# Optimization experiments

Hardware: AMD Instinct MI355X
Metric: run time of the kernel (lower is better)

Reference implementation:

```python
import jax, jax.numpy as jnp
import numpy as np

H_DIM = 256
N_HEADS = 8
HALF = H_DIM // 2

def _lin(x, W, b):
    # torch nn.Linear: y = x @ W.T + b
    y = x @ W.T
    return y + b if b is not None else y

def setup_inputs() -> dict:
    key = jax.random.key(0)
    ks = jax.random.split(key, 16)
    s = 0.02
    d = {
        'x': jax.random.normal(ks[0], (16, H_DIM, 32, 32), jnp.float32),
        'q1_w': jax.random.normal(ks[1], (HALF, HALF), jnp.float32) * s,
        'q1_b': jnp.zeros((HALF,), jnp.float32),
        'q2_w': jax.random.normal(ks[2], (HALF, HALF), jnp.float32) * s,
        'q2_b': jnp.zeros((HALF,), jnp.float32),
        'k1_w': jax.random.normal(ks[3], (HALF, HALF), jnp.float32) * s,
        'k1_b': jnp.zeros((HALF,), jnp.float32),
        'k2_w': jax.random.normal(ks[4], (HALF, HALF), jnp.float32) * s,
        'k2_b': jnp.zeros((HALF,), jnp.float32),
        'v1_w': jax.random.normal(ks[5], (HALF, HALF), jnp.float32) * s,
        'v1_b': jnp.zeros((HALF,), jnp.float32),
        'v2_w': jax.random.normal(ks[6], (HALF, HALF), jnp.float32) * s,
        'v2_b': jnp.zeros((HALF,), jnp.float32),
        'proj1_w': jax.random.normal(ks[7], (HALF, HALF), jnp.float32) * s,
        'proj1_b': jnp.zeros((HALF,), jnp.float32),
        'proj2_w': jax.random.normal(ks[8], (HALF, HALF), jnp.float32) * s,
        'proj2_b': jnp.zeros((HALF,), jnp.float32),
        'logit_scale': jnp.log(10.0 * jnp.ones((N_HEADS, 1, 1), jnp.float32)),
        'mlp_w1': jax.random.normal(ks[9], (128, 2), jnp.float32) * s,
        'mlp_b1': jnp.zeros((128,), jnp.float32),
        'mlp_w2': jax.random.normal(ks[10], (N_HEADS, 128), jnp.float32) * s,
    }
    return d

def _rel_pos_index(h, w):
    # static (numpy) relative position index, shape [N, N]
    ch, cw = np.meshgrid(np.arange(h), np.arange(w), indexing='ij')
    coords = np.stack([ch.reshape(-1), cw.reshape(-1)])  # [2, N]
    rel = coords[:, :, None] - coords[:, None, :]         # [2, N, N]
    rel = rel.transpose(1, 2, 0)
    rel[:, :, 0] += h - 1
    rel[:, :, 1] += w - 1
    return rel[:, :, 0] * (2 * w - 1) + rel[:, :, 1]

def _forward(x, q1_w, q1_b, q2_w, q2_b, k1_w, k1_b, k2_w, k2_b,
             v1_w, v1_b, v2_w, v2_b, proj1_w, proj1_b, proj2_w, proj2_b,
             logit_scale, mlp_w1, mlp_b1, mlp_w2):
    b, c, h, w = x.shape
    N = h * w
    nh = N_HEADS
    hd = c // nh
    x3 = jnp.transpose(x, (0, 2, 3, 1)).reshape(b, N, c)
    x0, x1 = x3[..., :c // 2], x3[..., c // 2:]

    def qkv(W0, b0, W1, b1):
        t = jnp.concatenate([x0 + _lin(x0, W0, b0), x1 + _lin(x1, W1, b1)], axis=-1)
        return t.reshape(b, N, nh, hd).transpose(0, 2, 1, 3)  # [b, nh, N, hd]

    q = qkv(q1_w, q1_b, q2_w, q2_b)
    k = qkv(k1_w, k1_b, k2_w, k2_b)
    v = qkv(v1_w, v1_b, v2_w, v2_b)

    eps = 1e-12
    qn = q / jnp.maximum(jnp.linalg.norm(q, axis=-1, keepdims=True), eps)
    kn = k / jnp.maximum(jnp.linalg.norm(k, axis=-1, keepdims=True), eps)
    attn = jnp.einsum('bhnd,bhmd->bhnm', qn, kn)  # cosine similarity
    scale = jnp.exp(jnp.minimum(logit_scale, jnp.log(1.0 / 0.01)))  # [nh,1,1]
    attn = attn * scale[None]

    # continuous relative-position bias (CPB) table via small MLP
    rch = jnp.arange(-(h - 1), h, dtype=jnp.float32) / (h - 1 + 1e-8)
    rcw = jnp.arange(-(w - 1), w, dtype=jnp.float32) / (w - 1 + 1e-8)
    gh, gw = jnp.meshgrid(rch, rcw, indexing='ij')
    tab = jnp.stack([gh, gw], axis=-1) * 3.2               # [2h-1, 2w-1, 2]
    tab = jnp.sign(tab) * (1.0 - jnp.exp(-jnp.abs(tab)))
    tab = jax.nn.relu(_lin(tab, mlp_w1, mlp_b1))
    tab = _lin(tab, mlp_w2, None).reshape(-1, nh)          # [(2h-1)(2w-1), nh]

    idx = jnp.asarray(_rel_pos_index(h, w))                # [N, N]
    bias = tab[idx.reshape(-1)].reshape(N, N, nh).transpose(2, 0, 1)
    bias = 16.0 * jax.nn.sigmoid(bias)
    attn = attn + bias[None]

    attn = jax.nn.softmax(attn, axis=-1)
    out = jnp.einsum('bhnm,bhmd->bhnd', attn, v).transpose(0, 2, 1, 3).reshape(b, N, c)
    o0, o1 = out[..., :c // 2], out[..., c // 2:]
    out = jnp.concatenate([_lin(o0, proj1_w, proj1_b), _lin(o1, proj2_w, proj2_b)], axis=-1)
    return out.reshape(b, h, w, c).transpose(0, 3, 1, 2)

def reference(x, q1_w, q1_b, q2_w, q2_b, k1_w, k1_b, k2_w, k2_b,
              v1_w, v1_b, v2_w, v2_b, proj1_w, proj1_b, proj2_w, proj2_b,
              logit_scale, mlp_w1, mlp_b1, mlp_w2):
    return _forward(x, q1_w, q1_b, q2_w, q2_b, k1_w, k1_b, k2_w, k2_b,
                    v1_w, v1_b, v2_w, v2_b, proj1_w, proj1_b, proj2_w, proj2_b,
                    logit_scale, mlp_w1, mlp_b1, mlp_w2)
```

## Files before the change

kernel.cpp:

```cpp
#include <hip/hip_runtime.h>
#include <cmath>


typedef _Float16 half_t;
typedef __attribute__((ext_vector_type(2))) __fp16 fp16x2;
typedef __attribute__((ext_vector_type(4))) _Float16 half4;
typedef __attribute__((ext_vector_type(8))) _Float16 half8;
typedef __attribute__((ext_vector_type(2))) float float2v;
typedef __attribute__((ext_vector_type(4))) float float4v;
typedef __attribute__((ext_vector_type(2))) unsigned int uint2v;

static __device__ __forceinline__ float4v mfma16(half8 a, half8 b, float4v c) {
  return __builtin_amdgcn_mfma_f32_16x16x32_f16(a, b, c, 0, 0, 0);
}

struct PtrArr8 { const float* p[8]; };

__global__ __launch_bounds__(256) void prep_w(PtrArr8 wsrc, PtrArr8 bsrc,
                                              half_t* __restrict__ wf,
                                              float* __restrict__ bws) {
  int y = blockIdx.y;
  const float* src = nullptr;
  const float* bs = nullptr;
#pragma unroll
  for (int i = 0; i < 8; i++)
    if (i == y) { src = wsrc.p[i]; bs = bsrc.p[i]; }
  int flat = (blockIdx.x * 256 + threadIdx.x) * 4;
  float4 w = *(const float4*)(src + flat);
  int j = flat >> 7, k = flat & 127;
  if (y < 6) {
    if (k == j)     w.x += 1.0f;
    if (k + 1 == j) w.y += 1.0f;
    if (k + 2 == j) w.z += 1.0f;
    if (k + 3 == j) w.w += 1.0f;
  }
  half4 h;
  h[0] = (half_t)w.x;
  h[1] = (half_t)w.y;
  h[2] = (half_t)w.z;
  h[3] = (half_t)w.w;
  int ng = j >> 4, l = j & 15, ks = k >> 5, quad = (k >> 3) & 3, o8 = k & 7;
  *(half4*)(wf + y * 16384 + ((ng * 4 + ks) * 64 + quad * 16 + l) * 8 + o8) =
      h;
  if (blockIdx.x == 0 && threadIdx.x < 128)
    bws[y * 128 + threadIdx.x] = bs[threadIdx.x];
}

__global__ __launch_bounds__(256) void bias_mlp(const float* __restrict__ w1,
                                                const float* __restrict__ b1,
                                                const float* __restrict__ w2,
                                                const float* __restrict__ ls,
                                                float* __restrict__ tabh2) {
  __shared__ float sw1[256];
  __shared__ float sb1[128];
  __shared__ float sw2[1024];
  int t = threadIdx.x;
  sw1[t] = w1[t];
  if (t < 128) sb1[t] = b1[t];
  for (int i = t; i < 1024; i += 256) sw2[i] = w2[i];
  __syncthreads();
  int p = blockIdx.x * 256 + t;
  if (p >= 3969) return;
  int ph = p / 63, pw = p % 63;
  float t0 = (float)(ph - 31) * (3.2f / 31.0f);
  float t1 = (float)(pw - 31) * (3.2f / 31.0f);
  t0 = copysignf(1.0f - __expf(-fabsf(t0)), t0);
  t1 = copysignf(1.0f - __expf(-fabsf(t1)), t1);
  float acc[8];
#pragma unroll
  for (int hh = 0; hh < 8; hh++) acc[hh] = 0.0f;
  for (int j = 0; j < 128; j++) {
    float hj = fmaxf(0.0f, t0 * sw1[2 * j] + t1 * sw1[2 * j + 1] + sb1[j]);
#pragma unroll
    for (int hh = 0; hh < 8; hh++) acc[hh] += hj * sw2[hh * 128 + j];
  }
  const float L2E = 1.44269504f;
#pragma unroll
  for (int hh = 0; hh < 8; hh++) {
    float scale = __expf(fminf(ls[hh], 4.6051702f));
    float c14 = 14.0f - (scale + 16.0f) * L2E;
    float bias = 16.0f / (1.0f + __expf(-acc[hh]));
    tabh2[hh * 3969 + p] = bias * L2E + c14;
  }
}

__global__ __launch_bounds__(256, 4) void qkv_mfma(
    const float* __restrict__ x, const half_t* __restrict__ wfrag,
    const float* __restrict__ lscale, const float* __restrict__ bws,
    half_t* __restrict__ qf, half_t* __restrict__ kf,
    half_t* __restrict__ vf) {
  __shared__ half_t tbuf[4608];
  int t = threadIdx.x;
  int lane = t & 63, wv = t >> 6, l = lane & 15, quad = lane >> 4;
  int rw = wv & 1, cw = wv >> 1;
  int hf = blockIdx.y;
  int m0 = blockIdx.x * 32;
  int b = m0 >> 10, n0 = m0 & 1023;

  half8 afr[4];
  {
    const float* xb =
        x + ((size_t)b * 256 + hf * 128) * 1024 + n0 + rw * 16 + l;
#pragma unroll
    for (int ks = 0; ks < 4; ks++) {
      half8 a;
#pragma unroll
      for (int j = 0; j < 8; j++)
        a[j] = (half_t)xb[(size_t)(ks * 32 + quad * 8 + j) * 1024];
      afr[ks] = a;
    }
  }

  for (int op = 0; op < 3; op++) {
    int combo = op * 2 + hf;
    const half_t* wfb = wfrag + combo * 16384;
    float4v acc[4];
#pragma unroll
    for (int ngl = 0; ngl < 4; ngl++) {
      int ng = cw * 4 + ngl;
      float4v c = {0.f, 0.f, 0.f, 0.f};
#pragma unroll
      for (int ks = 0; ks < 4; ks++) {
        half8 bfrag =
            *(const half8*)(wfb + ((ng * 4 + ks) * 64 + lane) * 8);
        c = mfma16(afr[ks], bfrag, c);
      }
      acc[ngl] = c;
    }
#pragma unroll
    for (int ngl = 0; ngl < 4; ngl++) {
      float bb = bws[combo * 128 + (cw * 4 + ngl) * 16 + l];
#pragma unroll
      for (int r2 = 0; r2 < 4; r2++) acc[ngl][r2] += bb;
    }
    if (op < 2) {
#pragma unroll
      for (int hgl = 0; hgl < 2; hgl++) {
        float sc = 1.0f;
        if (op == 0)
          sc = __expf(fminf(lscale[hf * 4 + cw * 2 + hgl], 4.6051702f)) *
               1.44269504f;
#pragma unroll
        for (int r2 = 0; r2 < 4; r2++) {
          float ss = acc[2 * hgl][r2] * acc[2 * hgl][r2] +
                     acc[2 * hgl + 1][r2] * acc[2 * hgl + 1][r2];
          ss += __shfl_xor(ss, 1, 64);
          ss += __shfl_xor(ss, 2, 64);
          ss += __shfl_xor(ss, 4, 64);
          ss += __shfl_xor(ss, 8, 64);
          float rn = sc / fmaxf(sqrtf(ss), 1e-12f);
          acc[2 * hgl][r2] *= rn;
          acc[2 * hgl + 1][r2] *= rn;
        }
      }
#pragma unroll
      for (int ngl = 0; ngl < 4; ngl++)
#pragma unroll
        for (int r2 = 0; r2 < 4; r2++)
          tbuf[(rw * 16 + quad * 4 + r2) * 136 + (cw * 4 + ngl) * 16 + l] =
              (half_t)acc[ngl][r2];
      __syncthreads();
      half_t* dst = (op == 0) ? qf : kf;
#pragma unroll
      for (int i = 0; i < 2; i++) {
        int idx = t + 256 * i;
        int row = idx >> 4, colc = (idx & 15) * 8;
        half8 vv = *(const half8*)(tbuf + row * 136 + colc);
        int head = hf * 4 + (colc >> 5), d = colc & 31;
        *(half8*)(dst + (((size_t)b * 8 + head) * 1024 + n0 + row) * 32 + d) =
            vv;
      }
      __syncthreads();
    } else {
#pragma unroll
      for (int ngl = 0; ngl < 4; ngl++) {
        int col = (cw * 4 + ngl) * 16 + l;
        half4 hv;
#pragma unroll
        for (int r2 = 0; r2 < 4; r2++) hv[r2] = (half_t)acc[ngl][r2];
        *(half4*)(tbuf + col * 36 + rw * 16 + quad * 4) = hv;
      }
      __syncthreads();
#pragma unroll
      for (int i = 0; i < 8; i++) {
        int idx = t + 256 * i;
        int col = idx >> 4, rp = idx & 15;
        unsigned int val = *(const unsigned int*)(tbuf + col * 36 + rp * 2);
        int head = hf * 4 + (col >> 5);
        int d = col & 31;
        *(unsigned int*)((char*)vf +
                         (((((size_t)b * 8 + head) * 32 + d) * 1024) + n0 +
                          rp * 2) * 2) = val;
      }
    }
  }
}


#define LOADKV(kt, VV)                                                      \
  {                                                                         \
    _Pragma("unroll") for (int nt = 0; nt < 4; nt++)                        \
        kfr[nt] = *(const half8*)(kbase + ((kt)*64 + nt * 16 + l) * 32 +    \
                                  quad * 8);                                \
    _Pragma("unroll") for (int ks = 0; ks < 2; ks++) {                      \
      VV[0][ks] = *(const half8*)(vbase + l * 1024 + (kt)*64 + ks * 32 +    \
                                  quad * 8);                                \
      VV[1][ks] = *(const half8*)(vbase + (16 + l) * 1024 + (kt)*64 +       \
                                  ks * 32 + quad * 8);                      \
    }                                                                       \
  }

#define QK_PHASE(kt, S, SR)                                                 \
  {                                                                         \
    int rowb = (wv + 31 - 2 * (kt)) * 63 + cA + (S)*16;                     \
    _Pragma("unroll") for (int nt = 0; nt < 4; nt++) {                      \
      int base = rowb - (nt >> 1) * 63 - (nt & 1) * 16;                     \
      float2v p0 = sb2d[base];                                              \
      float2v p1 = sb2d[base - 2];                                          \
      float4v c;                                                            \
      c[0] = p0[1];                                                         \
      c[1] = p0[0];                                                         \
      c[2] = p1[1];                                                         \
      c[3] = p1[0];                                                         \
      SR[nt] = mfma16(kfr[nt], qfr[S], c);                                  \
    }                                                                       \
  }

#define EXP_WRITE(S, SR)                                                    \
  {                                                                         \
    half_t* paws = pa + (wv * 2 + (S)) * 1152;                              \
    _Pragma("unroll") for (int nt = 0; nt < 4; nt++) {                      \
      fp16x2 plo = __builtin_amdgcn_cvt_pkrtz(exp2f(SR[nt][0]),             \
                                              exp2f(SR[nt][1]));            \
      fp16x2 phi = __builtin_amdgcn_cvt_pkrtz(exp2f(SR[nt][2]),             \
                                              exp2f(SR[nt][3]));            \
      uint2v uu;                                                            \
      uu.x = __builtin_bit_cast(unsigned int, plo);                         \
      uu.y = __builtin_bit_cast(unsigned int, phi);                         \
      *(uint2v*)(paws + l * 72 +                                            \
                 (((nt * 2 + (quad >> 1)) ^ pswz) << 3) +                   \
                 ((quad & 1) << 2)) = uu;                                   \
    }                                                                       \
  }

#define PV_PHASE(S, VV)                                                     \
  {                                                                         \
    const half_t* paws = pa + (wv * 2 + (S)) * 1152;                        \
    _Pragma("unroll") for (int ks = 0; ks < 2; ks++) {                      \
      half8 pfr = *(const half8*)(paws + l * 72 +                           \
                                  (((ks * 4 + quad) ^ pswz) << 3));         \
      o0[S] = mfma16(pfr, VV[0][ks], o0[S]);                                \
      o1[S] = mfma16(pfr, VV[1][ks], o1[S]);                                \
      accl[S] = mfma16(pfr, ones, accl[S]);                                 \
    }                                                                       \
  }

#define ITER(kt, VC, VN, DO_PREV, DO_PREF)                                  \
  {                                                                         \
    float4v sres[4];                                                        \
    QK_PHASE(kt, 0, sres);                                                  \
    if (DO_PREV) PV_PHASE(1, VN);                                           \
    EXP_WRITE(0, sres);                                                     \
    float4v sres2[4];                                                       \
    QK_PHASE(kt, 1, sres2);                                                 \
    if (DO_PREF) LOADKV((kt) + 1, VN);                                      \
    PV_PHASE(0, VC);                                                        \
    EXP_WRITE(1, sres2);                                                    \
  }

__global__ __launch_bounds__(256) void attn_mfma(
    const half_t* __restrict__ qf, const half_t* __restrict__ kf,
    const half_t* __restrict__ vf, const float* __restrict__ tabh2,
    half_t* __restrict__ ao) {
  __shared__ float2v sb2d[2205];
  __shared__ half_t pa[9216];

  int id = blockIdx.x;
  int qo = id >> 7;
  int bh = id & 127;
  int h = bh & 7, b = bh >> 3;
  int t = threadIdx.x;
  int lane = t & 63, wv = t >> 6, l = lane & 15, quad = lane >> 4;
  size_t bhs = (size_t)b * 8 + h;
  const half_t* kbase = kf + bhs * 1024 * 32;
  const half_t* vbase = vf + bhs * 32 * 1024;
  int row0 = qo * 128 + wv * 32;
  int cA = l + 31 - quad * 4;
  int pswz = (l >> 3) << 2;

  half8 kfr[4], va[2][2], vb[2][2], qfr[2];
  LOADKV(0, va);
#pragma unroll
  for (int s = 0; s < 2; s++)
    qfr[s] = *(const half8*)(qf + (bhs * 1024 + row0 + s * 16 + l) * 32 +
                             quad * 8);

  {
    const float* tb = tabh2 + h * 3969 + qo * 252;
    for (int i = t; i < 2205; i += 256) {
      float2v pr;
      pr[0] = (i > 0) ? tb[i - 1] : 0.0f;
      pr[1] = tb[i];
      sb2d[i] = pr;
    }
  }

  float4v o0[2], o1[2], accl[2];
#pragma unroll
  for (int s = 0; s < 2; s++) {
    o0[s] = (float4v){0.f, 0.f, 0.f, 0.f};
    o1[s] = (float4v){0.f, 0.f, 0.f, 0.f};
    accl[s] = (float4v){0.f, 0.f, 0.f, 0.f};
  }
  half8 ones;
#pragma unroll
  for (int j = 0; j < 8; j++) ones[j] = (half_t)1.0f;

  __syncthreads();

  ITER(0, va, vb, 0, 1);
  ITER(1, vb, va, 1, 1);
  for (int kt2 = 2; kt2 < 14; kt2 += 2) {
    ITER(kt2, va, vb, 1, 1);
    ITER(kt2 + 1, vb, va, 1, 1);
  }
  ITER(14, va, vb, 1, 1);
  ITER(15, vb, va, 1, 0);
  PV_PHASE(1, vb);

#pragma unroll
  for (int s = 0; s < 2; s++) {
#pragma unroll
    for (int r2 = 0; r2 < 4; r2++) {
      float linv = 1.0f / accl[s][r2];
      size_t rowaddr =
          ((size_t)b * 1024 + row0 + s * 16 + quad * 4 + r2) * 256 + h * 32;
      ao[rowaddr + l] = (half_t)(o0[s][r2] * linv);
      ao[rowaddr + 16 + l] = (half_t)(o1[s][r2] * linv);
    }
  }
}

__global__ __launch_bounds__(256, 4) void proj_mfma(
    const half_t* __restrict__ ao, const half_t* __restrict__ wfrag,
    const float* __restrict__ bws, float* __restrict__ out) {
  __shared__ float yt[128 * 36];
  int t = threadIdx.x;
  int lane = t & 63, wv = t >> 6, l = lane & 15, quad = lane >> 4;
  int rw = wv & 1, cw = wv >> 1;
  int hf = blockIdx.y;
  int m0 = blockIdx.x * 32;
  int b = m0 >> 10, n0 = m0 & 1023;

  half8 afr[4];
  const half_t* ab =
      ao + ((size_t)m0 + rw * 16 + l) * 256 + hf * 128 + quad * 8;
#pragma unroll
  for (int ks = 0; ks < 4; ks++) afr[ks] = *(const half8*)(ab + ks * 32);

  const half_t* wfb = wfrag + (6 + hf) * 16384;
#pragma unroll
  for (int ngl = 0; ngl < 4; ngl++) {
    int ng = cw * 4 + ngl;
    float4v c = {0.f, 0.f, 0.f, 0.f};
#pragma unroll
    for (int ks = 0; ks < 4; ks++) {
      half8 bfrag = *(const half8*)(wfb + ((ng * 4 + ks) * 64 + lane) * 8);
      c = mfma16(afr[ks], bfrag, c);
    }
    float bb = bws[(6 + hf) * 128 + ng * 16 + l];
#pragma unroll
    for (int r2 = 0; r2 < 4; r2++) c[r2] += bb;
    *(float4v*)(yt + (ng * 16 + l) * 36 + rw * 16 + quad * 4) = c;
  }
  __syncthreads();
#pragma unroll
  for (int i = 0; i < 4; i++) {
    int idx = t + 256 * i;
    int col = idx >> 3, rg = idx & 7;
    float4v vv = *(const float4v*)(yt + col * 36 + rg * 4);
    *(float4v*)(out + ((size_t)b * 256 + hf * 128 + col) * 1024 + n0 +
                rg * 4) = vv;
  }
}

extern "C" void kernel_launch(void* const* d_in, const int* in_sizes, int n_in,
                              void* d_out, int out_size, void* d_ws,
                              size_t ws_size, hipStream_t stream) {
  (void)in_sizes; (void)n_in; (void)out_size; (void)ws_size;
  const float* x = (const float*)d_in[0];

  half_t* ws = (half_t*)d_ws;
  half_t* qfp = ws;
  half_t* kfp = ws + 4194304;
  half_t* vfp = ws + 8388608;
  half_t* aop = ws + 12582912;
  half_t* wfp = ws + 16777216;
  float* tabh2 = (float*)((char*)d_ws + 33816576);
  float* bws = (float*)((char*)d_ws + 33943584);

  PtrArr8 wsrc, bsrc;
  const int widx[8] = {1, 3, 5, 7, 9, 11, 13, 15};
  for (int i = 0; i < 8; i++) {
    wsrc.p[i] = (const float*)d_in[widx[i]];
    bsrc.p[i] = (const float*)d_in[widx[i] + 1];
  }

  prep_w<<<dim3(16, 8), 256, 0, stream>>>(wsrc, bsrc, wfp, bws);
  bias_mlp<<<16, 256, 0, stream>>>((const float*)d_in[18],
                                   (const float*)d_in[19],
                                   (const float*)d_in[20],
                                   (const float*)d_in[17], tabh2);
  qkv_mfma<<<dim3(512, 2), 256, 0, stream>>>(x, wfp, (const float*)d_in[17],
                                             bws, qfp, kfp, vfp);
  attn_mfma<<<1024, 256, 0, stream>>>(qfp, kfp, vfp, tabh2, aop);
  proj_mfma<<<dim3(512, 2), 256, 0, stream>>>(aop, wfp, bws, (float*)d_out);
}
```

Measured before the change: 189.6 us.

## Keep attention probabilities in registers by permuting V layout to match MFMA output

V is now stored with the sequence dimension permuted so the QK^T MFMA accumulator layout can be fed straight back as the A operand of the PV MFMA. This removes the shared-memory round trip (write, then swizzled read) for the softmax probabilities and the pa LDS buffer. The main loop is restructured into a fully unrolled 16-step loop with separate K and V prefetch, dropping the double-buffered V registers and the interleaved software pipeline. That loss of QK/PV overlap, and the larger unrolled body, could raise register pressure or expose latency.

```diff
diff --git a/kernel.cpp b/kernel.cpp
--- a/kernel.cpp
+++ b/kernel.cpp
@@ -8,7 +8,7 @@
 typedef __attribute__((ext_vector_type(8))) _Float16 half8;
 typedef __attribute__((ext_vector_type(2))) float float2v;
 typedef __attribute__((ext_vector_type(4))) float float4v;
-typedef __attribute__((ext_vector_type(2))) unsigned int uint2v;
+typedef __attribute__((ext_vector_type(4))) unsigned int uint4v;
 
 static __device__ __forceinline__ float4v mfma16(half8 a, half8 b, float4v c) {
   return __builtin_amdgcn_mfma_f32_16x16x32_f16(a, b, c, 0, 0, 0);
@@ -181,6 +181,8 @@
         *(half4*)(tbuf + col * 36 + rw * 16 + quad * 4) = hv;
       }
       __syncthreads();
+      int p64 = (n0 >> 5) & 1;
+      int nb64 = n0 & ~63;
 #pragma unroll
       for (int i = 0; i < 8; i++) {
         int idx = t + 256 * i;
@@ -188,25 +190,31 @@
         unsigned int val = *(const unsigned int*)(tbuf + col * 36 + rp * 2);
         int head = hf * 4 + (col >> 5);
         int d = col & 31;
+        int npos = nb64 + ((rp >> 1) & 3) * 16 + (rp & 1) * 8 + p64 * 4 +
+                   ((rp >> 3) & 1) * 2;
         *(unsigned int*)((char*)vf +
-                         (((((size_t)b * 8 + head) * 32 + d) * 1024) + n0 +
-                          rp * 2) * 2) = val;
+                         (((((size_t)b * 8 + head) * 32 + d) * 1024) + npos) *
+                             2) = val;
       }
     }
   }
 }
 
 
-#define LOADKV(kt, VV)                                                      \
+#define LOADK(kt)                                                           \
   {                                                                         \
     _Pragma("unroll") for (int nt = 0; nt < 4; nt++)                        \
         kfr[nt] = *(const half8*)(kbase + ((kt)*64 + nt * 16 + l) * 32 +    \
                                   quad * 8);                                \
+  }
+
+#define LOADV(kt)                                                           \
+  {                                                                         \
     _Pragma("unroll") for (int ks = 0; ks < 2; ks++) {                      \
-      VV[0][ks] = *(const half8*)(vbase + l * 1024 + (kt)*64 + ks * 32 +    \
-                                  quad * 8);                                \
-      VV[1][ks] = *(const half8*)(vbase + (16 + l) * 1024 + (kt)*64 +       \
-                                  ks * 32 + quad * 8);                      \
+      vv0[ks] = *(const half8*)(vbase + l * 1024 + (kt)*64 + quad * 16 +    \
+                                ks * 8);                                    \
+      vv1[ks] = *(const half8*)(vbase + (16 + l) * 1024 + (kt)*64 +         \
+                                quad * 16 + ks * 8);                        \
     }                                                                       \
   }
 
@@ -226,46 +234,30 @@
     }                                                                       \
   }
 
-#define EXP_WRITE(S, SR)                                                    \
+#define EXP_PACK(S, SR)                                                     \
   {                                                                         \
-    half_t* paws = pa + (wv * 2 + (S)) * 1152;                              \
+    unsigned int w0[4], w1[4];                                              \
     _Pragma("unroll") for (int nt = 0; nt < 4; nt++) {                      \
       fp16x2 plo = __builtin_amdgcn_cvt_pkrtz(exp2f(SR[nt][0]),             \
                                               exp2f(SR[nt][1]));            \
       fp16x2 phi = __builtin_amdgcn_cvt_pkrtz(exp2f(SR[nt][2]),             \
                                               exp2f(SR[nt][3]));            \
-      uint2v uu;                                                            \
-      uu.x = __builtin_bit_cast(unsigned int, plo);                         \
-      uu.y = __builtin_bit_cast(unsigned int, phi);                         \
-      *(uint2v*)(paws + l * 72 +                                            \
-                 (((nt * 2 + (quad >> 1)) ^ pswz) << 3) +                   \
-                 ((quad & 1) << 2)) = uu;                                   \
+      w0[nt] = __builtin_bit_cast(unsigned int, plo);                       \
+      w1[nt] = __builtin_bit_cast(unsigned int, phi);                       \
     }                                                                       \
-  }
-
-#define PV_PHASE(S, VV)                                                     \
+    uint4v u0 = {w0[0], w0[1], w0[2], w0[3]};                               \
+    uint4v u1 = {w1[0], w1[1], w1[2], w1[3]};                               \
+    pf##S[0] = __builtin_bit_cast(half8, u0);                               \
+    pf##S[1] = __builtin_bit_cast(half8, u1);                               \
+  }
+
+#define PV_PHASE(S)                                                         \
   {                                                                         \
-    const half_t* paws = pa + (wv * 2 + (S)) * 1152;                        \
     _Pragma("unroll") for (int ks = 0; ks < 2; ks++) {                      \
-      half8 pfr = *(const half8*)(paws + l * 72 +                           \
-                                  (((ks * 4 + quad) ^ pswz) << 3));         \
-      o0[S] = mfma16(pfr, VV[0][ks], o0[S]);                                \
-      o1[S] = mfma16(pfr, VV[1][ks], o1[S]);                                \
-      accl[S] = mfma16(pfr, ones, accl[S]);                                 \
+      o0[S] = mfma16(pf##S[ks], vv0[ks], o0[S]);                            \
+      o1[S] = mfma16(pf##S[ks], vv1[ks], o1[S]);                            \
+      accl[S] = mfma16(pf##S[ks], ones, accl[S]);                           \
     }                                                                       \
-  }
-
-#define ITER(kt, VC, VN, DO_PREV, DO_PREF)                                  \
-  {                                                                         \
-    float4v sres[4];                                                        \
-    QK_PHASE(kt, 0, sres);                                                  \
-    if (DO_PREV) PV_PHASE(1, VN);                                           \
-    EXP_WRITE(0, sres);                                                     \
-    float4v sres2[4];                                                       \
-    QK_PHASE(kt, 1, sres2);                                                 \
-    if (DO_PREF) LOADKV((kt) + 1, VN);                                      \
-    PV_PHASE(0, VC);                                                        \
-    EXP_WRITE(1, sres2);                                                    \
   }
 
 __global__ __launch_bounds__(256) void attn_mfma(
@@ -273,7 +265,6 @@
     const half_t* __restrict__ vf, const float* __restrict__ tabh2,
     half_t* __restrict__ ao) {
   __shared__ float2v sb2d[2205];
-  __shared__ half_t pa[9216];
 
   int id = blockIdx.x;
   int qo = id >> 7;
@@ -286,10 +277,10 @@
   const half_t* vbase = vf + bhs * 32 * 1024;
   int row0 = qo * 128 + wv * 32;
   int cA = l + 31 - quad * 4;
-  int pswz = (l >> 3) << 2;
-
-  half8 kfr[4], va[2][2], vb[2][2], qfr[2];
-  LOADKV(0, va);
+
+  half8 kfr[4], vv0[2], vv1[2], qfr[2], pf0[2], pf1[2];
+  LOADK(0);
+  LOADV(0);
 #pragma unroll
   for (int s = 0; s < 2; s++)
     qfr[s] = *(const half8*)(qf + (bhs * 1024 + row0 + s * 16 + l) * 32 +
@@ -318,15 +309,19 @@
 
   __syncthreads();
 
-  ITER(0, va, vb, 0, 1);
-  ITER(1, vb, va, 1, 1);
-  for (int kt2 = 2; kt2 < 14; kt2 += 2) {
-    ITER(kt2, va, vb, 1, 1);
-    ITER(kt2 + 1, vb, va, 1, 1);
-  }
-  ITER(14, va, vb, 1, 1);
-  ITER(15, vb, va, 1, 0);
-  PV_PHASE(1, vb);
+#pragma unroll
+  for (int kt = 0; kt < 16; ++kt) {
+    float4v sres[4];
+    QK_PHASE(kt, 0, sres);
+    EXP_PACK(0, sres);
+    float4v sres2[4];
+    QK_PHASE(kt, 1, sres2);
+    if (kt < 15) LOADK(kt + 1);
+    EXP_PACK(1, sres2);
+    PV_PHASE(0);
+    PV_PHASE(1);
+    if (kt < 15) LOADV(kt + 1);
+  }
 
 #pragma unroll
   for (int s = 0; s < 2; s++) {
```

After: 190.9 us. No clear change (+0.7%).
